# Kernel tuning notes

Measured on AMD Instinct MI355X. Metric: run time of the kernel, lower is better.

## Reference

```python
import jax, jax.numpy as jnp
import numpy as np

D_MODEL = 1024
N_HEADS = 16


def setup_inputs() -> dict:
    key = jax.random.key(0)
    ks = jax.random.split(key, 11)
    B, S, D = 2, 2048, D_MODEL
    scale = 1.0 / np.sqrt(D)
    inp = {
        "q": jax.random.normal(ks[0], (B, S, D), jnp.float32),
        "k": jax.random.normal(ks[1], (B, S, D), jnp.float32),
        "v": jax.random.normal(ks[2], (B, S, D), jnp.float32),
        "W_q": jax.random.normal(ks[3], (D, D), jnp.float32) * scale,
        "b_q": jnp.zeros((D,), jnp.float32),
        "W_k": jax.random.normal(ks[4], (D, D), jnp.float32) * scale,
        "b_k": jnp.zeros((D,), jnp.float32),
        "W_v": jax.random.normal(ks[5], (D, D), jnp.float32) * scale,
        "b_v": jnp.zeros((D,), jnp.float32),
        "W_o": jax.random.normal(ks[6], (D, D), jnp.float32) * scale,
        "b_o": jnp.zeros((D,), jnp.float32),
    }
    return inp


def reference(q, k, v, W_q, b_q, W_k, b_k, W_v, b_v, W_o, b_o):
    B, S, D = q.shape
    H = N_HEADS
    d_k = D // H
    # linear projections, then split heads: [B, H, S, d_k]
    def proj(x, W, b):
        y = jnp.einsum("bsd,de->bse", x, W.T) + b
        return y.reshape(B, S, H, d_k).transpose(0, 2, 1, 3)
    Q = proj(q, W_q, b_q)
    K = proj(k, W_k, b_k)
    V = proj(v, W_v, b_v)
    # scaled dot-product attention with explicit [B,H,S,S] scores
    scores = jnp.einsum("bhqd,bhkd->bhqk", Q, K) / jnp.sqrt(jnp.float32(d_k))
    attn = jax.nn.softmax(scores, axis=-1)
    out = jnp.einsum("bhqk,bhkd->bhqd", attn, V)
    out = out.transpose(0, 2, 1, 3).reshape(B, S, D)
    return jnp.einsum("bsd,de->bse", out, W_o.T) + b_o
```

## Files before the change

### kernel.cpp

```cpp
#include <hip/hip_runtime.h>
#include <hip/hip_bf16.h>
#include <math.h>

typedef __bf16 bf16_t;
typedef bf16_t bf16x8 __attribute__((ext_vector_type(8)));
typedef float f32x4 __attribute__((ext_vector_type(4)));

#define D_MODEL 1024
#define NH 16
#define DK 64
#define SEQ 2048
#define MROWS 4096
#define LDSW 64
#define LDC 136

__device__ __forceinline__ bf16x8 ldfrag(const bf16_t* p) {
    union { uint4 u; bf16x8 v; } c;
    c.u = *reinterpret_cast<const uint4*>(p);
    return c.v;
}

__device__ __forceinline__ f32x4 zero4() { f32x4 z = {0.f, 0.f, 0.f, 0.f}; return z; }

__device__ __forceinline__ void gll16(const bf16_t* g, bf16_t* l) {
    __builtin_amdgcn_global_load_lds(
        (const __attribute__((address_space(1))) unsigned int*)g,
        (__attribute__((address_space(3))) unsigned int*)l,
        16, 0, 0);
}

__global__ void pack7(const float* __restrict__ q, const float* __restrict__ k,
                      const float* __restrict__ v, const float* __restrict__ wq,
                      const float* __restrict__ wk, const float* __restrict__ wv,
                      const float* __restrict__ wo,
                      bf16_t* __restrict__ dq, bf16_t* __restrict__ dk,
                      bf16_t* __restrict__ dv, bf16_t* __restrict__ dwq,
                      bf16_t* __restrict__ dwk, bf16_t* __restrict__ dwv,
                      bf16_t* __restrict__ dwo) {
    const int y = blockIdx.y;
    if (y >= 3 && blockIdx.x >= 512) return;
    const float* s;
    bf16_t* d;
    switch (y) {
        case 0: s = q;  d = dq;  break;
        case 1: s = k;  d = dk;  break;
        case 2: s = v;  d = dv;  break;
        case 3: s = wq; d = dwq; break;
        case 4: s = wk; d = dwk; break;
        case 5: s = wv; d = dwv; break;
        default: s = wo; d = dwo; break;
    }
    int i = (blockIdx.x * blockDim.x + threadIdx.x) * 8;
    float4 f0 = *reinterpret_cast<const float4*>(s + i);
    float4 f1 = *reinterpret_cast<const float4*>(s + i + 4);
    union { bf16_t h[8]; uint4 u; } o;
    o.h[0] = (bf16_t)f0.x; o.h[1] = (bf16_t)f0.y; o.h[2] = (bf16_t)f0.z; o.h[3] = (bf16_t)f0.w;
    o.h[4] = (bf16_t)f1.x; o.h[5] = (bf16_t)f1.y; o.h[6] = (bf16_t)f1.z; o.h[7] = (bf16_t)f1.w;
    *reinterpret_cast<uint4*>(d + i) = o.u;
}

__device__ __forceinline__ void gemm_core(
    const bf16_t* __restrict__ A, const bf16_t* __restrict__ Bm,
    int K, int m0, int n0,
    bf16_t* As, bf16_t* Bs,
    f32x4 acc[4][4]) {

    const int tid = threadIdx.x;
    const int lane = tid & 63;
    const int wid = tid >> 6;
    const int wm = (wid >> 1) * 64, wn = (wid & 1) * 64;
    const int l15 = lane & 15, quad = lane >> 4;

    const int lrow   = lane >> 3;
    const int gcol   = ((lane & 7) ^ lrow) * 8;

    #pragma unroll
    for (int i = 0; i < 4; i++)
        #pragma unroll
        for (int j = 0; j < 4; j++) acc[i][j] = zero4();

    for (int k0 = 0; k0 < K; k0 += 64) {
        __syncthreads();
        #pragma unroll
        for (int t = 0; t < 4; t++) {
            const int rbase = wid * 32 + t * 8;
            gll16(A  + (size_t)(m0 + rbase + lrow) * K + k0 + gcol, As + rbase * LDSW);
            gll16(Bm + (size_t)(n0 + rbase + lrow) * K + k0 + gcol, Bs + rbase * LDSW);
        }
        __syncthreads();
        #pragma unroll
        for (int c = 0; c < 2; c++) {
            bf16x8 af[4], bfr[4];
            #pragma unroll
            for (int i = 0; i < 4; i++) {
                const int row = wm + i * 16 + l15;
                const int pc = ((c * 4 + quad) ^ (l15 & 7)) * 8;
                af[i] = ldfrag(As + row * LDSW + pc);
            }
            #pragma unroll
            for (int j = 0; j < 4; j++) {
                const int row = wn + j * 16 + l15;
                const int pc = ((c * 4 + quad) ^ (l15 & 7)) * 8;
                bfr[j] = ldfrag(Bs + row * LDSW + pc);
            }
            #pragma unroll
            for (int i = 0; i < 4; i++)
                #pragma unroll
                for (int j = 0; j < 4; j++)
                    acc[i][j] = __builtin_amdgcn_mfma_f32_16x16x32_bf16(af[i], bfr[j], acc[i][j], 0, 0, 0);
        }
    }
}

__global__ __launch_bounds__(256, 3) void proj_gemm(
    const bf16_t* __restrict__ qb, const bf16_t* __restrict__ kb,
    const bf16_t* __restrict__ vb,
    const bf16_t* __restrict__ Wq, const bf16_t* __restrict__ Wk,
    const bf16_t* __restrict__ Wv,
    const float* __restrict__ bq, const float* __restrict__ bk, const float* __restrict__ bv,
    bf16_t* __restrict__ Qh, bf16_t* __restrict__ Kh, bf16_t* __restrict__ Vt) {

    __shared__ __align__(16) bf16_t sm[128 * LDC];
    bf16_t* As = sm;
    bf16_t* Bs = sm + 128 * LDSW;
    bf16_t (*Cs)[LDC] = reinterpret_cast<bf16_t(*)[LDC]>(sm);
    f32x4 acc[4][4];

    const int mode = blockIdx.z;
    const bf16_t* X = (mode == 0) ? qb : (mode == 1) ? kb : vb;
    const bf16_t* W = (mode == 0) ? Wq : (mode == 1) ? Wk : Wv;
    const float* bias = (mode == 0) ? bq : (mode == 1) ? bk : bv;
    const int m0 = blockIdx.y * 128, n0 = blockIdx.x * 128;

    gemm_core(X, W, D_MODEL, m0, n0, As, Bs, acc);

    const int tid = threadIdx.x, lane = tid & 63, wid = tid >> 6;
    const int wm = (wid >> 1) * 64, wn = (wid & 1) * 64;
    const int l15 = lane & 15, quad = lane >> 4;

    __syncthreads();
    if (mode != 2) {
        const float sc = (mode == 0) ? 0.125f * 1.44269504f : 1.0f;
        #pragma unroll
        for (int i = 0; i < 4; i++)
            #pragma unroll
            for (int j = 0; j < 4; j++)
                #pragma unroll
                for (int r = 0; r < 4; r++) {
                    int gn = n0 + wn + j * 16 + l15;
                    Cs[wm + i * 16 + quad * 4 + r][wn + j * 16 + l15] =
                        (bf16_t)((acc[i][j][r] + bias[gn]) * sc);
                }
    } else {
        #pragma unroll
        for (int i = 0; i < 4; i++)
            #pragma unroll
            for (int j = 0; j < 4; j++)
                #pragma unroll
                for (int r = 0; r < 4; r++) {
                    int gn = n0 + wn + j * 16 + l15;
                    Cs[wn + j * 16 + l15][wm + i * 16 + quad * 4 + r] =
                        (bf16_t)(acc[i][j][r] + bias[gn]);
                }
    }
    __syncthreads();

    #pragma unroll
    for (int c = tid; c < 2048; c += 256) {
        int row = c >> 4, col8 = (c & 15) << 3;
        uint4 val = *reinterpret_cast<const uint4*>(&Cs[row][col8]);
        if (mode != 2) {
            int gm = m0 + row, gn = n0 + col8;
            int b = gm >> 11, seq = gm & 2047;
            int h = gn >> 6, dk = gn & 63;
            bf16_t* dst = (mode == 0) ? Qh : Kh;
            *reinterpret_cast<uint4*>(dst + ((size_t)(b * NH + h) * SEQ + seq) * DK + dk) = val;
        } else {
            int gn = n0 + row, gm = m0 + col8;
            int b = gm >> 11, seq = gm & 2047;
            int h = gn >> 6, dk = gn & 63;
            *reinterpret_cast<uint4*>(Vt + ((size_t)(b * NH + h) * DK + dk) * SEQ + seq) = val;
        }
    }
}

__global__ __launch_bounds__(256, 2) void out_gemm(
    const bf16_t* __restrict__ Oc, const bf16_t* __restrict__ Wo,
    const float* __restrict__ bo, float* __restrict__ Cout) {

    __shared__ __align__(16) bf16_t As[64 * LDSW];
    __shared__ __align__(16) bf16_t Bs[128 * LDSW];
    f32x4 acc[2][4];
    const int m0 = blockIdx.y * 64, n0 = blockIdx.x * 128;

    const int tid = threadIdx.x;
    const int lane = tid & 63;
    const int wid = tid >> 6;
    const int wm = (wid >> 1) * 32, wn = (wid & 1) * 64;
    const int l15 = lane & 15, quad = lane >> 4;
    const int lrow = lane >> 3;
    const int gcol = ((lane & 7) ^ lrow) * 8;

    #pragma unroll
    for (int i = 0; i < 2; i++)
        #pragma unroll
        for (int j = 0; j < 4; j++) acc[i][j] = zero4();

    for (int k0 = 0; k0 < D_MODEL; k0 += 64) {
        __syncthreads();
        #pragma unroll
        for (int t = 0; t < 2; t++) {
            const int rbase = wid * 16 + t * 8;
            gll16(Oc + (size_t)(m0 + rbase + lrow) * D_MODEL + k0 + gcol, As + rbase * LDSW);
        }
        #pragma unroll
        for (int t = 0; t < 4; t++) {
            const int rbase = wid * 32 + t * 8;
            gll16(Wo + (size_t)(n0 + rbase + lrow) * D_MODEL + k0 + gcol, Bs + rbase * LDSW);
        }
        __syncthreads();
        #pragma unroll
        for (int c = 0; c < 2; c++) {
            bf16x8 af[2], bfr[4];
            #pragma unroll
            for (int i = 0; i < 2; i++) {
                const int row = wm + i * 16 + l15;
                const int pc = ((c * 4 + quad) ^ (l15 & 7)) * 8;
                af[i] = ldfrag(As + row * LDSW + pc);
            }
            #pragma unroll
            for (int j = 0; j < 4; j++) {
                const int row = wn + j * 16 + l15;
                const int pc = ((c * 4 + quad) ^ (l15 & 7)) * 8;
                bfr[j] = ldfrag(Bs + row * LDSW + pc);
            }
            #pragma unroll
            for (int i = 0; i < 2; i++)
                #pragma unroll
                for (int j = 0; j < 4; j++)
                    acc[i][j] = __builtin_amdgcn_mfma_f32_16x16x32_bf16(af[i], bfr[j], acc[i][j], 0, 0, 0);
        }
    }

    #pragma unroll
    for (int i = 0; i < 2; i++)
        #pragma unroll
        for (int j = 0; j < 4; j++)
            #pragma unroll
            for (int r = 0; r < 4; r++) {
                int gm = m0 + wm + i * 16 + quad * 4 + r;
                int gn = n0 + wn + j * 16 + l15;
                Cout[(size_t)gm * D_MODEL + gn] = acc[i][j][r] + bo[gn];
            }
}

__global__ __launch_bounds__(512, 4) void attn_kernel(
    const bf16_t* __restrict__ Qh, const bf16_t* __restrict__ Kh,
    const bf16_t* __restrict__ Vt, bf16_t* __restrict__ Oc) {

    __shared__ __align__(16) bf16_t sma[16384];
    bf16_t* Ks  = sma;
    bf16_t* Vts = sma + 128 * 64;
    bf16_t* Pls = sma;

    const int tid = threadIdx.x, lane = tid & 63, wid = tid >> 6;
    const int l15 = lane & 15, quad = lane >> 4;
    const int bh = blockIdx.x;
    const int q0 = blockIdx.y * 128;
    const bf16_t* Qbase = Qh + (size_t)bh * SEQ * DK;
    const bf16_t* Kbase = Kh + (size_t)bh * SEQ * DK;
    const bf16_t* Vbase = Vt + (size_t)bh * DK * SEQ;

    const int lrow = lane >> 3;
    const int gcol = ((lane & 7) ^ lrow) * 8;

    bf16x8 aQ[2];
    #pragma unroll
    for (int c = 0; c < 2; c++)
        aQ[c] = ldfrag(Qbase + (size_t)(q0 + wid * 16 + l15) * DK + c * 32 + quad * 8);

    f32x4 oacc[4];
    #pragma unroll
    for (int j = 0; j < 4; j++) oacc[j] = zero4();
    float l_acc = 0.f;

    const int s7 = l15 & 7;
    const int vlrow = lane >> 4;
    const int vchk0 = lane & 15;

    for (int kt = 0; kt < SEQ / 128; kt++) {
        const int k0 = kt * 128;
        __syncthreads();
        #pragma unroll
        for (int t = 0; t < 2; t++) {
            const int rbase = wid * 16 + t * 8;
            const int srow = rbase + lrow;
            const int sigma = ((srow >> 5) << 5) | (((srow >> 2) & 3) << 3) |
                              (((srow >> 4) & 1) << 2) | (srow & 3);
            gll16(Kbase + (size_t)(k0 + sigma) * DK + gcol, Ks + rbase * 64);

            const int vrb = wid * 8 + t * 4;
            const int vrow = vrb + vlrow;
            gll16(Vbase + (size_t)vrow * SEQ + k0 + ((vchk0 ^ (vrow & 15)) << 3),
                  Vts + vrb * 128);
        }
        __syncthreads();

        f32x4 sacc[8];
        #pragma unroll
        for (int j = 0; j < 8; j++) sacc[j] = zero4();
        #pragma unroll
        for (int c = 0; c < 2; c++) {
            bf16x8 bk4[8];
            #pragma unroll
            for (int j = 0; j < 8; j++) {
                const int pc = ((c * 4 + quad) ^ s7) * 8;
                bk4[j] = ldfrag(Ks + (j * 16 + l15) * 64 + pc);
            }
            #pragma unroll
            for (int j = 0; j < 8; j++)
                sacc[j] = __builtin_amdgcn_mfma_f32_16x16x32_bf16(
                    bk4[j], aQ[c], sacc[j], 0, 0, 0);
        }

        bf16x8 pb[4];
        #pragma unroll
        for (int c = 0; c < 4; c++) {
            union { bf16_t h[8]; bf16x8 v; } pk;
            #pragma unroll
            for (int half = 0; half < 2; half++) {
                const int j = c * 2 + half;
                float e0 = exp2f(sacc[j][0]);
                float e1 = exp2f(sacc[j][1]);
                float e2 = exp2f(sacc[j][2]);
                float e3 = exp2f(sacc[j][3]);
                l_acc += (e0 + e1) + (e2 + e3);
                pk.h[half * 4 + 0] = (bf16_t)e0;
                pk.h[half * 4 + 1] = (bf16_t)e1;
                pk.h[half * 4 + 2] = (bf16_t)e2;
                pk.h[half * 4 + 3] = (bf16_t)e3;
            }
            pb[c] = pk.v;
        }

        #pragma unroll
        for (int c = 0; c < 4; c++) {
            bf16x8 av[4];
            #pragma unroll
            for (int j = 0; j < 4; j++) {
                const int pc = ((c * 4 + quad) ^ l15) * 8;
                av[j] = ldfrag(Vts + (j * 16 + l15) * 128 + pc);
            }
            #pragma unroll
            for (int j = 0; j < 4; j++)
                oacc[j] = __builtin_amdgcn_mfma_f32_16x16x32_bf16(
                    av[j], pb[c], oacc[j], 0, 0, 0);
        }
    }

    float l = l_acc;
    l += __shfl_xor(l, 16, 64);
    l += __shfl_xor(l, 32, 64);
    const float inv = 1.0f / l;

    __syncthreads();

    bf16_t* orow = Pls + (wid * 16 + l15) * LDSW;
    #pragma unroll
    for (int jp = 0; jp < 4; jp++) {
        union { bf16_t h[4]; unsigned long long u; } pk;
        pk.h[0] = (bf16_t)(oacc[jp][0] * inv);
        pk.h[1] = (bf16_t)(oacc[jp][1] * inv);
        pk.h[2] = (bf16_t)(oacc[jp][2] * inv);
        pk.h[3] = (bf16_t)(oacc[jp][3] * inv);
        const int Lc = jp * 2 + (quad >> 1);
        *reinterpret_cast<unsigned long long*>(
            orow + ((Lc ^ s7) << 3) + ((quad & 1) << 2)) = pk.u;
    }
    __syncthreads();

    const int b = bh >> 4, h = bh & 15;
    #pragma unroll
    for (int c = tid; c < 1024; c += 512) {
        int row = c >> 3, chunk = c & 7;
        uint4 val = *reinterpret_cast<const uint4*>(
            Pls + row * LDSW + ((chunk ^ (row & 7)) << 3));
        *reinterpret_cast<uint4*>(Oc + ((size_t)(b * SEQ + q0 + row)) * D_MODEL + h * DK + (chunk << 3)) = val;
    }
}

extern "C" void kernel_launch(void* const* d_in, const int* in_sizes, int n_in,
                              void* d_out, int out_size, void* d_ws, size_t ws_size,
                              hipStream_t stream) {
    const float* q  = (const float*)d_in[0];
    const float* k  = (const float*)d_in[1];
    const float* v  = (const float*)d_in[2];
    const float* Wq = (const float*)d_in[3];
    const float* bq = (const float*)d_in[4];
    const float* Wk = (const float*)d_in[5];
    const float* bk = (const float*)d_in[6];
    const float* Wv = (const float*)d_in[7];
    const float* bv = (const float*)d_in[8];
    const float* Wo = (const float*)d_in[9];
    const float* bo = (const float*)d_in[10];

    const size_t nx = (size_t)MROWS * D_MODEL;
    const size_t nw = (size_t)D_MODEL * D_MODEL;

    bf16_t* qb  = (bf16_t*)d_ws;
    bf16_t* kb  = qb  + nx;
    bf16_t* vb  = kb  + nx;
    bf16_t* Wqb = vb  + nx;
    bf16_t* Wkb = Wqb + nw;
    bf16_t* Wvb = Wkb + nw;
    bf16_t* Wob = Wvb + nw;
    bf16_t* Qh  = Wob + nw;
    bf16_t* Kh  = Qh  + nx;
    bf16_t* Vt  = Kh  + nx;
    bf16_t* Oc  = Vt  + nx;

    pack7<<<dim3(2048, 7), 256, 0, stream>>>(q, k, v, Wq, Wk, Wv, Wo,
                                             qb, kb, vb, Wqb, Wkb, Wvb, Wob);

    proj_gemm<<<dim3(8, 32, 3), 256, 0, stream>>>(qb, kb, vb, Wqb, Wkb, Wvb, bq, bk, bv, Qh, Kh, Vt);
    attn_kernel<<<dim3(32, 16), 512, 0, stream>>>(Qh, Kh, Vt, Oc);
    out_gemm<<<dim3(8, 64), 256, 0, stream>>>(Oc, Wob, bo, (float*)d_out);
}
```

Measured before the change: 220.4 us.

## Double the attention key tile and compute row sums with an MFMA

The attention kernel now processes 256 keys per iteration instead of 128, using twice the LDS, which halves the number of barrier-separated load phases. The softmax denominator is no longer a scalar accumulation plus cross-lane shuffles. It is computed by an extra MFMA that multiplies a vector of ones by the bf16 probabilities, so the sum uses the same rounded values as the PV product. The cost is more LDS per block, which may lower occupancy, more live registers (16 score accumulators), and extra MFMA work for the sum.

Measured after the change: 270.6 us. 22.8% more time.

```diff
diff --git a/kernel.cpp b/kernel.cpp
--- a/kernel.cpp
+++ b/kernel.cpp
@@ -258,9 +258,9 @@
     const bf16_t* __restrict__ Qh, const bf16_t* __restrict__ Kh,
     const bf16_t* __restrict__ Vt, bf16_t* __restrict__ Oc) {
 
-    __shared__ __align__(16) bf16_t sma[16384];
+    __shared__ __align__(16) bf16_t sma[32768];
     bf16_t* Ks  = sma;
-    bf16_t* Vts = sma + 128 * 64;
+    bf16_t* Vts = sma + 256 * 64;
     bf16_t* Pls = sma;
 
     const int tid = threadIdx.x, lane = tid & 63, wid = tid >> 6;
@@ -279,89 +279,78 @@
     for (int c = 0; c < 2; c++)
         aQ[c] = ldfrag(Qbase + (size_t)(q0 + wid * 16 + l15) * DK + c * 32 + quad * 8);
 
+    bf16x8 aOne;
+    {
+        union { bf16_t h[8]; bf16x8 v; } u1;
+        #pragma unroll
+        for (int i = 0; i < 8; i++) u1.h[i] = (bf16_t)1.0f;
+        aOne = u1.v;
+    }
+
     f32x4 oacc[4];
     #pragma unroll
     for (int j = 0; j < 4; j++) oacc[j] = zero4();
-    float l_acc = 0.f;
+    f32x4 lsum = zero4();
 
     const int s7 = l15 & 7;
-    const int vlrow = lane >> 4;
-    const int vchk0 = lane & 15;
-
-    for (int kt = 0; kt < SEQ / 128; kt++) {
-        const int k0 = kt * 128;
-        __syncthreads();
-        #pragma unroll
-        for (int t = 0; t < 2; t++) {
-            const int rbase = wid * 16 + t * 8;
+    const int vlrow = lane >> 5;
+    const int vchk0 = lane & 31;
+
+    for (int kt = 0; kt < SEQ / 256; kt++) {
+        const int k0 = kt * 256;
+        __syncthreads();
+        #pragma unroll
+        for (int t = 0; t < 4; t++) {
+            const int rbase = wid * 32 + t * 8;
             const int srow = rbase + lrow;
             const int sigma = ((srow >> 5) << 5) | (((srow >> 2) & 3) << 3) |
                               (((srow >> 4) & 1) << 2) | (srow & 3);
             gll16(Kbase + (size_t)(k0 + sigma) * DK + gcol, Ks + rbase * 64);
 
-            const int vrb = wid * 8 + t * 4;
+            const int vrb = wid * 8 + t * 2;
             const int vrow = vrb + vlrow;
-            gll16(Vbase + (size_t)vrow * SEQ + k0 + ((vchk0 ^ (vrow & 15)) << 3),
-                  Vts + vrb * 128);
-        }
-        __syncthreads();
-
-        f32x4 sacc[8];
-        #pragma unroll
-        for (int j = 0; j < 8; j++) sacc[j] = zero4();
-        #pragma unroll
-        for (int c = 0; c < 2; c++) {
-            bf16x8 bk4[8];
-            #pragma unroll
-            for (int j = 0; j < 8; j++) {
-                const int pc = ((c * 4 + quad) ^ s7) * 8;
-                bk4[j] = ldfrag(Ks + (j * 16 + l15) * 64 + pc);
-            }
-            #pragma unroll
-            for (int j = 0; j < 8; j++)
-                sacc[j] = __builtin_amdgcn_mfma_f32_16x16x32_bf16(
-                    bk4[j], aQ[c], sacc[j], 0, 0, 0);
-        }
-
-        bf16x8 pb[4];
-        #pragma unroll
-        for (int c = 0; c < 4; c++) {
+            gll16(Vbase + (size_t)vrow * SEQ + k0 + ((vchk0 ^ (vrow & 31)) << 3),
+                  Vts + vrb * 256);
+        }
+        __syncthreads();
+
+        f32x4 sacc[16];
+        #pragma unroll
+        for (int j = 0; j < 16; j++) sacc[j] = zero4();
+        #pragma unroll
+        for (int j = 0; j < 16; j++) {
+            const bf16_t* krow = Ks + (j * 16 + l15) * 64;
+            bf16x8 b0 = ldfrag(krow + ((quad ^ s7) << 3));
+            bf16x8 b1 = ldfrag(krow + (((4 + quad) ^ s7) << 3));
+            sacc[j] = __builtin_amdgcn_mfma_f32_16x16x32_bf16(b0, aQ[0], sacc[j], 0, 0, 0);
+            sacc[j] = __builtin_amdgcn_mfma_f32_16x16x32_bf16(b1, aQ[1], sacc[j], 0, 0, 0);
+        }
+
+        #pragma unroll
+        for (int c = 0; c < 8; c++) {
             union { bf16_t h[8]; bf16x8 v; } pk;
             #pragma unroll
             for (int half = 0; half < 2; half++) {
                 const int j = c * 2 + half;
-                float e0 = exp2f(sacc[j][0]);
-                float e1 = exp2f(sacc[j][1]);
-                float e2 = exp2f(sacc[j][2]);
-                float e3 = exp2f(sacc[j][3]);
-                l_acc += (e0 + e1) + (e2 + e3);
-                pk.h[half * 4 + 0] = (bf16_t)e0;
-                pk.h[half * 4 + 1] = (bf16_t)e1;
-                pk.h[half * 4 + 2] = (bf16_t)e2;
-                pk.h[half * 4 + 3] = (bf16_t)e3;
-            }
-            pb[c] = pk.v;
-        }
-
-        #pragma unroll
-        for (int c = 0; c < 4; c++) {
-            bf16x8 av[4];
-            #pragma unroll
-            for (int j = 0; j < 4; j++) {
-                const int pc = ((c * 4 + quad) ^ l15) * 8;
-                av[j] = ldfrag(Vts + (j * 16 + l15) * 128 + pc);
-            }
-            #pragma unroll
-            for (int j = 0; j < 4; j++)
-                oacc[j] = __builtin_amdgcn_mfma_f32_16x16x32_bf16(
-                    av[j], pb[c], oacc[j], 0, 0, 0);
-        }
-    }
-
-    float l = l_acc;
-    l += __shfl_xor(l, 16, 64);
-    l += __shfl_xor(l, 32, 64);
-    const float inv = 1.0f / l;
+                pk.h[half * 4 + 0] = (bf16_t)exp2f(sacc[j][0]);
+                pk.h[half * 4 + 1] = (bf16_t)exp2f(sacc[j][1]);
+                pk.h[half * 4 + 2] = (bf16_t)exp2f(sacc[j][2]);
+                pk.h[half * 4 + 3] = (bf16_t)exp2f(sacc[j][3]);
+            }
+            const bf16x8 pb = pk.v;
+
+            lsum = __builtin_amdgcn_mfma_f32_16x16x32_bf16(aOne, pb, lsum, 0, 0, 0);
+
+            #pragma unroll
+            for (int jp = 0; jp < 4; jp++) {
+                const int row = jp * 16 + l15;
+                bf16x8 av = ldfrag(Vts + row * 256 + (((c * 4 + quad) ^ (row & 31)) << 3));
+                oacc[jp] = __builtin_amdgcn_mfma_f32_16x16x32_bf16(av, pb, oacc[jp], 0, 0, 0);
+            }
+        }
+    }
+
+    const float inv = 1.0f / lsum[0];
 
     __syncthreads();
 
```
